# Kernel tuning notes

Measured on AMD Instinct MI355X. Metric: run time of the kernel, lower is better.

## Reference

```python
import jax, jax.numpy as jnp
import numpy as np

B, L, C, H = 2, 2048, 1024, 16
D = C // H  # dim per head

def setup_inputs() -> dict:
    key = jax.random.key(0)
    ks = jax.random.split(key, 13)
    s = 1.0 / np.sqrt(C)
    inp = {
        "query": jax.random.normal(ks[0], (B, L, C), jnp.float32),
        "key": jax.random.normal(ks[1], (B, L, C), jnp.float32),
        "value": jax.random.normal(ks[2], (B, L, C), jnp.float32),
        "mask": jax.random.randint(ks[3], (B, 1, L, L), 0, 2, jnp.int32),
        "WQ": jax.random.normal(ks[4], (C, C), jnp.float32) * s,
        "bQ": jnp.zeros((C,), jnp.float32),
        "WK": jax.random.normal(ks[5], (C, C), jnp.float32) * s,
        "bK": jnp.zeros((C,), jnp.float32),
        "WV": jax.random.normal(ks[6], (C, C), jnp.float32) * s,
        "bV": jnp.zeros((C,), jnp.float32),
        "WO": jax.random.normal(ks[7], (C, C), jnp.float32) * s,
        "bO": jnp.zeros((C,), jnp.float32),
    }
    return inp

def reference(query, key, value, mask, WQ, bQ, WK, bK, WV, bV, WO, bO):
    b = query.shape[0]
    # projections: x @ W + b  (W stored [in, out])
    Q = query @ WQ + bQ
    K = key @ WK + bK
    V = value @ WV + bV
    # [B, L, C] -> [B, H, L, D]
    def split_heads(x):
        return x.reshape(b, -1, H, D).transpose(0, 2, 1, 3)
    Qh, Kh, Vh = split_heads(Q), split_heads(K), split_heads(V)
    scores = jnp.einsum("bhqd,bhkd->bhqk", Qh, Kh) / jnp.sqrt(jnp.float32(D))
    scores = jnp.where(mask == 0, jnp.float32(-1e9), scores)
    attn = jax.nn.softmax(scores, axis=-1)
    Z = jnp.einsum("bhqk,bhkd->bhqd", attn, Vh)  # [B, H, L, D]
    Z = Z.transpose(0, 2, 1, 3).reshape(b, Q.shape[1], C)
    return Z @ WO + bO
```

## Files before the change

kernel.cpp:

```cpp
#include <hip/hip_runtime.h>

#define BB 2
#define LL 2048
#define CC 1024
#define HH 16
#define DD 64
#define MM (BB * LL)

typedef __bf16 bf16x8 __attribute__((ext_vector_type(8)));
typedef float  f32x4  __attribute__((ext_vector_type(4)));

#define LOG2E 1.44269504088896340736f
#if defined(__has_builtin)
#if __has_builtin(__builtin_amdgcn_exp2f)
#define EXP2F(x) __builtin_amdgcn_exp2f(x)
#else
#define EXP2F(x) exp2f(x)
#endif
#else
#define EXP2F(x) exp2f(x)
#endif

__device__ __forceinline__ unsigned short f2bf(float x) {
    return __builtin_bit_cast(unsigned short, (__bf16)x);
}
__device__ __forceinline__ void split2(float x, unsigned short& hi, unsigned short& lo) {
    __bf16 h = (__bf16)x;
    hi = __builtin_bit_cast(unsigned short, h);
    lo = __builtin_bit_cast(unsigned short, (__bf16)(x - (float)h));
}

#define GLOAD_LDS16(g, l)                                                      \
    __builtin_amdgcn_global_load_lds(                                          \
        (const __attribute__((address_space(1))) void*)(g),                    \
        (__attribute__((address_space(3))) void*)(l), 16, 0, 0)

#define MFMA16(a, b, c) __builtin_amdgcn_mfma_f32_16x16x32_bf16((a), (b), (c), 0, 0, 0)

__global__ __launch_bounds__(256) void w_prep(
    const float* __restrict__ W, unsigned short* __restrict__ Whi,
    unsigned short* __restrict__ Wlo)
{
    __shared__ float T[64][65];
    const int tid = threadIdx.x;
    const int k0 = blockIdx.x * 64, n0 = blockIdx.y * 64;
    #pragma unroll
    for (int p = 0; p < 4; ++p) {
        const int idx = tid + p * 256;
        const int r = idx >> 4, c4 = idx & 15;
        float4 v = *(const float4*)&W[(size_t)(k0 + r) * CC + n0 + c4 * 4];
        T[r][c4 * 4 + 0] = v.x; T[r][c4 * 4 + 1] = v.y;
        T[r][c4 * 4 + 2] = v.z; T[r][c4 * 4 + 3] = v.w;
    }
    __syncthreads();
    #pragma unroll
    for (int p = 0; p < 16; ++p) {
        const int idx = tid + p * 256;
        const int n = idx >> 6, k = idx & 63;
        unsigned short hi, lo;
        split2(T[k][n], hi, lo);
        Whi[(size_t)(n0 + n) * CC + k0 + k] = hi;
        Wlo[(size_t)(n0 + n) * CC + k0 + k] = lo;
    }
}

__global__ __launch_bounds__(256) void x_prep(
    const float* __restrict__ X, unsigned short* __restrict__ Xhi,
    unsigned short* __restrict__ Xlo)
{
    const size_t i = (size_t)blockIdx.x * 256 + threadIdx.x;
    float4 v = *(const float4*)&X[i * 4];
    unsigned short h0, l0, h1, l1, h2, l2, h3, l3;
    split2(v.x, h0, l0); split2(v.y, h1, l1);
    split2(v.z, h2, l2); split2(v.w, h3, l3);
    ushort4 hv; hv.x = h0; hv.y = h1; hv.z = h2; hv.w = h3;
    ushort4 lv; lv.x = l0; lv.y = l1; lv.z = l2; lv.w = l3;
    *(ushort4*)&Xhi[i * 4] = hv;
    *(ushort4*)&Xlo[i * 4] = lv;
}

__global__ __launch_bounds__(256) void vt_prep(
    const float* __restrict__ Vp, unsigned short* __restrict__ Vt)
{
    __shared__ float T[64][65];
    const int tid = threadIdx.x;
    const int t = blockIdx.x, h = blockIdx.y, b = blockIdx.z;
    #pragma unroll
    for (int p = 0; p < 4; ++p) {
        const int idx = tid + p * 256;
        const int r = idx >> 4, c4 = idx & 15;
        float4 v = *(const float4*)&Vp[(size_t)(b * LL + t * 64 + r) * CC + h * DD + c4 * 4];
        T[r][c4 * 4 + 0] = v.x; T[r][c4 * 4 + 1] = v.y;
        T[r][c4 * 4 + 2] = v.z; T[r][c4 * 4 + 3] = v.w;
    }
    __syncthreads();
    unsigned short* out = Vt + (size_t)(b * HH + h) * DD * LL;
    #pragma unroll
    for (int p = 0; p < 16; ++p) {
        const int idx = tid + p * 256;
        const int d = idx >> 6, l = idx & 63;
        out[(size_t)d * LL + t * 64 + l] = f2bf(T[l][d]);
    }
}

__global__ __launch_bounds__(256) void mask_pack(
    const int* __restrict__ mask, unsigned int* __restrict__ mp)
{
    const size_t wi = (size_t)blockIdx.x * 256 + threadIdx.x;
    const int* src = mask + wi * 32;
    unsigned int v = 0;
    #pragma unroll
    for (int j = 0; j < 32; j += 4) {
        int4 m4 = *(const int4*)&src[j];
        if (m4.x != 0) v |= 1u << (j + 0);
        if (m4.y != 0) v |= 1u << (j + 1);
        if (m4.z != 0) v |= 1u << (j + 2);
        if (m4.w != 0) v |= 1u << (j + 3);
    }
    mp[wi] = v;
}

template <int MODE>
__global__ __launch_bounds__(256) void gemm_split(
    const unsigned short* __restrict__ Ahi, const unsigned short* __restrict__ Alo,
    const unsigned short* __restrict__ Bhi, const unsigned short* __restrict__ Blo,
    const float* __restrict__ bias, float scale,
    float* __restrict__ Yf,
    unsigned short* __restrict__ Yhi, unsigned short* __restrict__ Ylo)
{
    __shared__ __align__(16) unsigned short Ah[2][128 * 32];
    __shared__ __align__(16) unsigned short Al[2][128 * 32];
    __shared__ __align__(16) unsigned short Bh[2][128 * 32];
    __shared__ __align__(16) unsigned short Bl[2][128 * 32];

    const int tid  = threadIdx.x;
    const int lane = tid & 63, w = tid >> 6;
    const int wr = w >> 1, wc = w & 1;
    const int lr = lane & 15, kg = lane >> 4;
    const int row0 = blockIdx.x * 128, col0 = blockIdx.y * 128;

    f32x4 acc[4][4];
    #pragma unroll
    for (int i = 0; i < 4; ++i)
        #pragma unroll
        for (int j = 0; j < 4; ++j)
            acc[i][j] = (f32x4){0.f, 0.f, 0.f, 0.f};

    const int srow = lane >> 2;
    const int ssl  = ((lane & 3) ^ ((srow >> 1) & 3)) * 8;

    #define GSTAGE(bufi, kt_)                                                  \
        {                                                                      \
            const int k0_ = (kt_) * 32;                                        \
            _Pragma("unroll")                                                  \
            for (int c = 0; c < 2; ++c) {                                      \
                const int chunk = w * 2 + c;                                   \
                const int r = chunk * 16 + srow;                               \
                GLOAD_LDS16(Ahi + (size_t)(row0 + r) * CC + k0_ + ssl, &Ah[bufi][chunk * 512]); \
                GLOAD_LDS16(Alo + (size_t)(row0 + r) * CC + k0_ + ssl, &Al[bufi][chunk * 512]); \
                GLOAD_LDS16(Bhi + (size_t)(col0 + r) * CC + k0_ + ssl, &Bh[bufi][chunk * 512]); \
                GLOAD_LDS16(Blo + (size_t)(col0 + r) * CC + k0_ + ssl, &Bl[bufi][chunk * 512]); \
            }                                                                  \
        }

    GSTAGE(0, 0);
    __syncthreads();

    const int NT = CC / 32;
    for (int kt = 0; kt < NT; ++kt) {
        const int cur = kt & 1;
        if (kt + 1 < NT) GSTAGE(cur ^ 1, kt + 1);

        bf16x8 ah[4], al[4], bh[4], bl[4];
        const int ko = (kg ^ ((lr >> 1) & 3)) * 8;
        #pragma unroll
        for (int i = 0; i < 4; ++i) {
            ah[i] = *(const bf16x8*)&Ah[cur][(wr * 64 + i * 16 + lr) * 32 + ko];
            al[i] = *(const bf16x8*)&Al[cur][(wr * 64 + i * 16 + lr) * 32 + ko];
            bh[i] = *(const bf16x8*)&Bh[cur][(wc * 64 + i * 16 + lr) * 32 + ko];
            bl[i] = *(const bf16x8*)&Bl[cur][(wc * 64 + i * 16 + lr) * 32 + ko];
        }
        #pragma unroll
        for (int i = 0; i < 4; ++i)
            #pragma unroll
            for (int j = 0; j < 4; ++j) {
                acc[i][j] = MFMA16(ah[i], bh[j], acc[i][j]);
                acc[i][j] = MFMA16(ah[i], bl[j], acc[i][j]);
                acc[i][j] = MFMA16(al[i], bh[j], acc[i][j]);
            }
        __syncthreads();
    }
    #undef GSTAGE

    #pragma unroll
    for (int j = 0; j < 4; ++j) {
        const int n = col0 + wc * 64 + j * 16 + lr;
        const float bv = bias[n];
        #pragma unroll
        for (int i = 0; i < 4; ++i) {
            const int mbase = row0 + wr * 64 + i * 16 + kg * 4;
            #pragma unroll
            for (int r = 0; r < 4; ++r) {
                const float v = (acc[i][j][r] + bv) * scale;
                const int m = mbase + r;
                if (MODE == 0) {
                    Yf[(size_t)m * CC + n] = v;
                } else {
                    const int bb = m >> 11, ll = m & (LL - 1);
                    const int hh = n >> 6, dd = n & 63;
                    const size_t o = ((size_t)(bb * HH + hh) * LL + ll) * DD + dd;
                    unsigned short hi, lo;
                    split2(v, hi, lo);
                    Yhi[o] = hi; Ylo[o] = lo;
                }
            }
        }
    }
}

__global__ __launch_bounds__(256) void flash_mfma(
    const unsigned short* __restrict__ Qhi, const unsigned short* __restrict__ Qlo,
    const unsigned short* __restrict__ Khi, const unsigned short* __restrict__ Klo,
    const unsigned short* __restrict__ Vt,  const unsigned int* __restrict__ maskp,
    unsigned short* __restrict__ Zhi, unsigned short* __restrict__ Zlo)
{
    __shared__ __align__(16) unsigned short Kh_s[2][64 * 64];
    __shared__ __align__(16) unsigned short Kl_s[2][64 * 64];
    __shared__ __align__(16) unsigned short Vt_s[2][64 * 64];
    __shared__ __align__(16) __bf16 Ps[4][16 * 72];

    const int tid  = threadIdx.x;
    const int lane = tid & 63, w = tid >> 6;
    const int lr = lane & 15, kg = lane >> 4;
    const int q0 = blockIdx.x * 64;
    const int h = blockIdx.y, b = blockIdx.z;
    const size_t bh = (size_t)(b * HH + h);

    const unsigned short* Qhi_b = Qhi + bh * LL * DD;
    const unsigned short* Qlo_b = Qlo + bh * LL * DD;
    const unsigned short* Khi_b = Khi + bh * LL * DD;
    const unsigned short* Klo_b = Klo + bh * LL * DD;
    const unsigned short* Vt_b  = Vt  + bh * DD * LL;

    const int qrow = q0 + w * 16 + lr;
    bf16x8 qh[2], ql[2];
    #pragma unroll
    for (int s = 0; s < 2; ++s) {
        qh[s] = *(const bf16x8*)&Qhi_b[(size_t)qrow * DD + s * 32 + kg * 8];
        ql[s] = *(const bf16x8*)&Qlo_b[(size_t)qrow * DD + s * 32 + kg * 8];
    }

    f32x4 oacc[4];
    float m_r[4], l_r[4];
    #pragma unroll
    for (int r = 0; r < 4; ++r) {
        oacc[r] = (f32x4){0.f, 0.f, 0.f, 0.f};
        m_r[r] = -3.0e38f; l_r[r] = 0.f;
    }

    #define FSTAGE(bufi, kt_)                                                  \
        {                                                                      \
            _Pragma("unroll")                                                  \
            for (int c = 0; c < 2; ++c) {                                      \
                const int chunk = w * 2 + c;                                   \
                const int rowi = chunk * 8 + (lane >> 3);                      \
                const int cb   = (lane & 7) * 16;                              \
                const int scb  = cb ^ ((rowi & 7) << 4);                       \
                GLOAD_LDS16(Khi_b + (size_t)((kt_) * 64 + rowi) * DD + scb / 2, &Kh_s[bufi][chunk * 512]); \
                GLOAD_LDS16(Klo_b + (size_t)((kt_) * 64 + rowi) * DD + scb / 2, &Kl_s[bufi][chunk * 512]); \
                GLOAD_LDS16(Vt_b + (size_t)rowi * LL + (kt_) * 64 + scb / 2,    &Vt_s[bufi][chunk * 512]); \
            }                                                                  \
        }

    FSTAGE(0, 0);
    __syncthreads();

    const int NT = LL / 64;
    for (int kt = 0; kt < NT; ++kt) {
        const int cur = kt & 1;
        if (kt + 1 < NT) FSTAGE(cur ^ 1, kt + 1);

        f32x4 sacc[4];
        #pragma unroll
        for (int j = 0; j < 4; ++j) sacc[j] = (f32x4){0.f, 0.f, 0.f, 0.f};
        __builtin_amdgcn_s_setprio(1);
        #pragma unroll
        for (int j = 0; j < 4; ++j) {
            const int krow = j * 16 + lr;
            const int rswz = (krow & 7) << 4;
            #pragma unroll
            for (int s = 0; s < 2; ++s) {
                const int cb = (s * 64 + kg * 16) ^ rswz;
                bf16x8 kh = *(const bf16x8*)((const char*)&Kh_s[cur][0] + krow * 128 + cb);
                bf16x8 kl = *(const bf16x8*)((const char*)&Kl_s[cur][0] + krow * 128 + cb);
                sacc[j] = MFMA16(qh[s], kh, sacc[j]);
                sacc[j] = MFMA16(qh[s], kl, sacc[j]);
                sacc[j] = MFMA16(ql[s], kh, sacc[j]);
            }
        }
        __builtin_amdgcn_s_setprio(0);

        float mxr[4];
        #pragma unroll
        for (int r = 0; r < 4; ++r) {
            const int qr = q0 + w * 16 + kg * 4 + r;
            const unsigned int* mb = maskp + ((size_t)b * LL + qr) * (LL / 32) + kt * 2;
            const unsigned int m0 = mb[0], m1 = mb[1];
            float mx = -3.0e38f;
            #pragma unroll
            for (int j = 0; j < 4; ++j) {
                const unsigned int wsel = (j < 2) ? m0 : m1;
                const int bit = (j & 1) * 16 + lr;
                if (((wsel >> bit) & 1u) == 0u) sacc[j][r] = -1.0e9f;
                mx = fmaxf(mx, sacc[j][r]);
            }
            #pragma unroll
            for (int off = 1; off < 16; off <<= 1)
                mx = fmaxf(mx, __shfl_xor(mx, off, 16));
            mxr[r] = mx;
        }

        const float g = fmaxf(fmaxf(mxr[0] - m_r[0], mxr[1] - m_r[1]),
                              fmaxf(mxr[2] - m_r[2], mxr[3] - m_r[3]));
        if (!__all(g <= 8.0f)) {
            #pragma unroll
            for (int r = 0; r < 4; ++r) {
                const float mnew = fmaxf(m_r[r], mxr[r]);
                const float f = EXP2F(m_r[r] - mnew);
                m_r[r] = mnew;
                l_r[r] *= f;
                #pragma unroll
                for (int jd = 0; jd < 4; ++jd) oacc[jd][r] *= f;
            }
        }

        #pragma unroll
        for (int r = 0; r < 4; ++r) {
            float sum = 0.f;
            #pragma unroll
            for (int j = 0; j < 4; ++j) {
                const float p = EXP2F(sacc[j][r] - m_r[r]);
                sum += p;
                Ps[w][(kg * 4 + r) * 72 + j * 16 + lr] = (__bf16)p;
            }
            #pragma unroll
            for (int off = 1; off < 16; off <<= 1)
                sum += __shfl_xor(sum, off, 16);
            l_r[r] += sum;
        }

        __builtin_amdgcn_s_setprio(1);
        #pragma unroll
        for (int s = 0; s < 2; ++s) {
            bf16x8 pa = *(const bf16x8*)&Ps[w][lr * 72 + s * 32 + kg * 8];
            #pragma unroll
            for (int jd = 0; jd < 4; ++jd) {
                const int vrow = jd * 16 + lr;
                const int cb = (s * 64 + kg * 16) ^ ((vrow & 7) << 4);
                bf16x8 vb = *(const bf16x8*)((const char*)&Vt_s[cur][0] + vrow * 128 + cb);
                oacc[jd] = MFMA16(pa, vb, oacc[jd]);
            }
        }
        __builtin_amdgcn_s_setprio(0);
        __syncthreads();
    }
    #undef FSTAGE

    #pragma unroll
    for (int r = 0; r < 4; ++r) {
        const float inv = 1.0f / l_r[r];
        const int qg = q0 + w * 16 + kg * 4 + r;
        const size_t rowb = ((size_t)(b * LL + qg)) * CC + h * DD;
        #pragma unroll
        for (int jd = 0; jd < 4; ++jd) {
            unsigned short hi, lo;
            split2(oacc[jd][r] * inv, hi, lo);
            Zhi[rowb + jd * 16 + lr] = hi;
            Zlo[rowb + jd * 16 + lr] = lo;
        }
    }
}

extern "C" void kernel_launch(void* const* d_in, const int* in_sizes, int n_in,
                              void* d_out, int out_size, void* d_ws, size_t ws_size,
                              hipStream_t stream)
{
    const float* query = (const float*)d_in[0];
    const float* key   = (const float*)d_in[1];
    const float* value = (const float*)d_in[2];
    const int*   mask  = (const int*)d_in[3];
    const float* WQ = (const float*)d_in[4];
    const float* bQ = (const float*)d_in[5];
    const float* WK = (const float*)d_in[6];
    const float* bK = (const float*)d_in[7];
    const float* WV = (const float*)d_in[8];
    const float* bV = (const float*)d_in[9];
    const float* WO = (const float*)d_in[10];
    const float* bO = (const float*)d_in[11];
    float* out = (float*)d_out;

    char* ws = (char*)d_ws;
    const size_t MB = 1024 * 1024;
    unsigned short* WQt_hi = (unsigned short*)(ws + 0 * MB);
    unsigned short* WQt_lo = (unsigned short*)(ws + 2 * MB);
    unsigned short* WKt_hi = (unsigned short*)(ws + 4 * MB);
    unsigned short* WKt_lo = (unsigned short*)(ws + 6 * MB);
    unsigned short* WVt_hi = (unsigned short*)(ws + 8 * MB);
    unsigned short* WVt_lo = (unsigned short*)(ws + 10 * MB);
    unsigned short* WOt_hi = (unsigned short*)(ws + 12 * MB);
    unsigned short* WOt_lo = (unsigned short*)(ws + 14 * MB);
    unsigned short* Xhi    = (unsigned short*)(ws + 16 * MB);
    unsigned short* Xlo    = (unsigned short*)(ws + 24 * MB);
    unsigned short* Qh_hi  = (unsigned short*)(ws + 32 * MB);
    unsigned short* Qh_lo  = (unsigned short*)(ws + 40 * MB);
    unsigned short* Kh_hi  = (unsigned short*)(ws + 48 * MB);
    unsigned short* Kh_lo  = (unsigned short*)(ws + 56 * MB);
    float*          Vp     = (float*)(ws + 64 * MB);
    unsigned short* Vt     = (unsigned short*)(ws + 80 * MB);
    unsigned int*   maskp  = (unsigned int*)(ws + 88 * MB);

    const dim3 blk(256);
    const dim3 wgrid(CC / 64, CC / 64);
    w_prep<<<wgrid, blk, 0, stream>>>(WQ, WQt_hi, WQt_lo);
    w_prep<<<wgrid, blk, 0, stream>>>(WK, WKt_hi, WKt_lo);
    w_prep<<<wgrid, blk, 0, stream>>>(WV, WVt_hi, WVt_lo);
    w_prep<<<wgrid, blk, 0, stream>>>(WO, WOt_hi, WOt_lo);
    mask_pack<<<dim3((BB * LL * (LL / 32)) / 256), blk, 0, stream>>>(mask, maskp);

    const dim3 ggrid(MM / 128, CC / 128);
    const dim3 xgrid((size_t)MM * CC / 4 / 256);

    x_prep<<<xgrid, blk, 0, stream>>>(query, Xhi, Xlo);
    gemm_split<1><<<ggrid, blk, 0, stream>>>(Xhi, Xlo, WQt_hi, WQt_lo, bQ,
                                             0.125f * LOG2E, nullptr, Qh_hi, Qh_lo);
    x_prep<<<xgrid, blk, 0, stream>>>(key, Xhi, Xlo);
    gemm_split<1><<<ggrid, blk, 0, stream>>>(Xhi, Xlo, WKt_hi, WKt_lo, bK, 1.0f,
                                             nullptr, Kh_hi, Kh_lo);
    x_prep<<<xgrid, blk, 0, stream>>>(value, Xhi, Xlo);
    gemm_split<0><<<ggrid, blk, 0, stream>>>(Xhi, Xlo, WVt_hi, WVt_lo, bV, 1.0f,
                                             Vp, nullptr, nullptr);
    vt_prep<<<dim3(LL / 64, HH, BB), blk, 0, stream>>>(Vp, Vt);

    flash_mfma<<<dim3(LL / 64, HH, BB), blk, 0, stream>>>(
        Qh_hi, Qh_lo, Kh_hi, Kh_lo, Vt, maskp, Xhi, Xlo);

    gemm_split<0><<<ggrid, blk, 0, stream>>>(Xhi, Xlo, WOt_hi, WOt_lo, bO, 1.0f,
                                             out, nullptr, nullptr);
}
```

Baseline: 523.4 us.

## Replace double-buffered LDS staging with single-buffer load-sync-compute loops

Removes the double-buffered prefetch in both the split-bf16 GEMM and the flash attention kernel. Each iteration now loads its tile into a single LDS buffer, synchronizes, then computes. This halves LDS use per block, which may allow more resident blocks per CU. In exchange, global-to-LDS loads no longer overlap with MFMA compute inside a block, so the kernels rely on occupancy to hide memory latency.

```diff
diff --git a/kernel.cpp b/kernel.cpp
--- a/kernel.cpp
+++ b/kernel.cpp
@@ -128,10 +128,10 @@
     float* __restrict__ Yf,
     unsigned short* __restrict__ Yhi, unsigned short* __restrict__ Ylo)
 {
-    __shared__ __align__(16) unsigned short Ah[2][128 * 32];
-    __shared__ __align__(16) unsigned short Al[2][128 * 32];
-    __shared__ __align__(16) unsigned short Bh[2][128 * 32];
-    __shared__ __align__(16) unsigned short Bl[2][128 * 32];
+    __shared__ __align__(16) unsigned short Ah[128 * 32];
+    __shared__ __align__(16) unsigned short Al[128 * 32];
+    __shared__ __align__(16) unsigned short Bh[128 * 32];
+    __shared__ __align__(16) unsigned short Bl[128 * 32];
 
     const int tid  = threadIdx.x;
     const int lane = tid & 63, w = tid >> 6;
@@ -148,37 +148,29 @@
 
     const int srow = lane >> 2;
     const int ssl  = ((lane & 3) ^ ((srow >> 1) & 3)) * 8;
-
-    #define GSTAGE(bufi, kt_)                                                  \
-        {                                                                      \
-            const int k0_ = (kt_) * 32;                                        \
-            _Pragma("unroll")                                                  \
-            for (int c = 0; c < 2; ++c) {                                      \
-                const int chunk = w * 2 + c;                                   \
-                const int r = chunk * 16 + srow;                               \
-                GLOAD_LDS16(Ahi + (size_t)(row0 + r) * CC + k0_ + ssl, &Ah[bufi][chunk * 512]); \
-                GLOAD_LDS16(Alo + (size_t)(row0 + r) * CC + k0_ + ssl, &Al[bufi][chunk * 512]); \
-                GLOAD_LDS16(Bhi + (size_t)(col0 + r) * CC + k0_ + ssl, &Bh[bufi][chunk * 512]); \
-                GLOAD_LDS16(Blo + (size_t)(col0 + r) * CC + k0_ + ssl, &Bl[bufi][chunk * 512]); \
-            }                                                                  \
-        }
-
-    GSTAGE(0, 0);
-    __syncthreads();
+    const int ko   = (kg ^ ((lr >> 1) & 3)) * 8;
 
     const int NT = CC / 32;
     for (int kt = 0; kt < NT; ++kt) {
-        const int cur = kt & 1;
-        if (kt + 1 < NT) GSTAGE(cur ^ 1, kt + 1);
+        const int k0 = kt * 32;
+        #pragma unroll
+        for (int c = 0; c < 2; ++c) {
+            const int chunk = w * 2 + c;
+            const int r = chunk * 16 + srow;
+            GLOAD_LDS16(Ahi + (size_t)(row0 + r) * CC + k0 + ssl, &Ah[chunk * 512]);
+            GLOAD_LDS16(Alo + (size_t)(row0 + r) * CC + k0 + ssl, &Al[chunk * 512]);
+            GLOAD_LDS16(Bhi + (size_t)(col0 + r) * CC + k0 + ssl, &Bh[chunk * 512]);
+            GLOAD_LDS16(Blo + (size_t)(col0 + r) * CC + k0 + ssl, &Bl[chunk * 512]);
+        }
+        __syncthreads();
 
         bf16x8 ah[4], al[4], bh[4], bl[4];
-        const int ko = (kg ^ ((lr >> 1) & 3)) * 8;
         #pragma unroll
         for (int i = 0; i < 4; ++i) {
-            ah[i] = *(const bf16x8*)&Ah[cur][(wr * 64 + i * 16 + lr) * 32 + ko];
-            al[i] = *(const bf16x8*)&Al[cur][(wr * 64 + i * 16 + lr) * 32 + ko];
-            bh[i] = *(const bf16x8*)&Bh[cur][(wc * 64 + i * 16 + lr) * 32 + ko];
-            bl[i] = *(const bf16x8*)&Bl[cur][(wc * 64 + i * 16 + lr) * 32 + ko];
+            ah[i] = *(const bf16x8*)&Ah[(wr * 64 + i * 16 + lr) * 32 + ko];
+            al[i] = *(const bf16x8*)&Al[(wr * 64 + i * 16 + lr) * 32 + ko];
+            bh[i] = *(const bf16x8*)&Bh[(wc * 64 + i * 16 + lr) * 32 + ko];
+            bl[i] = *(const bf16x8*)&Bl[(wc * 64 + i * 16 + lr) * 32 + ko];
         }
         #pragma unroll
         for (int i = 0; i < 4; ++i)
@@ -190,7 +182,6 @@
             }
         __syncthreads();
     }
-    #undef GSTAGE
 
     #pragma unroll
     for (int j = 0; j < 4; ++j) {
@@ -224,9 +215,9 @@
     const unsigned short* __restrict__ Vt,  const unsigned int* __restrict__ maskp,
     unsigned short* __restrict__ Zhi, unsigned short* __restrict__ Zlo)
 {
-    __shared__ __align__(16) unsigned short Kh_s[2][64 * 64];
-    __shared__ __align__(16) unsigned short Kl_s[2][64 * 64];
-    __shared__ __align__(16) unsigned short Vt_s[2][64 * 64];
+    __shared__ __align__(16) unsigned short Kh_s[64 * 64];
+    __shared__ __align__(16) unsigned short Kl_s[64 * 64];
+    __shared__ __align__(16) unsigned short Vt_s[64 * 64];
     __shared__ __align__(16) __bf16 Ps[4][16 * 72];
 
     const int tid  = threadIdx.x;
@@ -258,27 +249,19 @@
         m_r[r] = -3.0e38f; l_r[r] = 0.f;
     }
 
-    #define FSTAGE(bufi, kt_)                                                  \
-        {                                                                      \
-            _Pragma("unroll")                                                  \
-            for (int c = 0; c < 2; ++c) {                                      \
-                const int chunk = w * 2 + c;                                   \
-                const int rowi = chunk * 8 + (lane >> 3);                      \
-                const int cb   = (lane & 7) * 16;                              \
-                const int scb  = cb ^ ((rowi & 7) << 4);                       \
-                GLOAD_LDS16(Khi_b + (size_t)((kt_) * 64 + rowi) * DD + scb / 2, &Kh_s[bufi][chunk * 512]); \
-                GLOAD_LDS16(Klo_b + (size_t)((kt_) * 64 + rowi) * DD + scb / 2, &Kl_s[bufi][chunk * 512]); \
-                GLOAD_LDS16(Vt_b + (size_t)rowi * LL + (kt_) * 64 + scb / 2,    &Vt_s[bufi][chunk * 512]); \
-            }                                                                  \
-        }
-
-    FSTAGE(0, 0);
-    __syncthreads();
-
     const int NT = LL / 64;
     for (int kt = 0; kt < NT; ++kt) {
-        const int cur = kt & 1;
-        if (kt + 1 < NT) FSTAGE(cur ^ 1, kt + 1);
+        #pragma unroll
+        for (int c = 0; c < 2; ++c) {
+            const int chunk = w * 2 + c;
+            const int rowi = chunk * 8 + (lane >> 3);
+            const int cb   = (lane & 7) * 16;
+            const int scb  = cb ^ ((rowi & 7) << 4);
+            GLOAD_LDS16(Khi_b + (size_t)(kt * 64 + rowi) * DD + scb / 2, &Kh_s[chunk * 512]);
+            GLOAD_LDS16(Klo_b + (size_t)(kt * 64 + rowi) * DD + scb / 2, &Kl_s[chunk * 512]);
+            GLOAD_LDS16(Vt_b + (size_t)rowi * LL + kt * 64 + scb / 2,    &Vt_s[chunk * 512]);
+        }
+        __syncthreads();
 
         f32x4 sacc[4];
         #pragma unroll
@@ -291,8 +274,8 @@
             #pragma unroll
             for (int s = 0; s < 2; ++s) {
                 const int cb = (s * 64 + kg * 16) ^ rswz;
-                bf16x8 kh = *(const bf16x8*)((const char*)&Kh_s[cur][0] + krow * 128 + cb);
-                bf16x8 kl = *(const bf16x8*)((const char*)&Kl_s[cur][0] + krow * 128 + cb);
+                bf16x8 kh = *(const bf16x8*)((const char*)&Kh_s[0] + krow * 128 + cb);
+                bf16x8 kl = *(const bf16x8*)((const char*)&Kl_s[0] + krow * 128 + cb);
                 sacc[j] = MFMA16(qh[s], kh, sacc[j]);
                 sacc[j] = MFMA16(qh[s], kl, sacc[j]);
                 sacc[j] = MFMA16(ql[s], kh, sacc[j]);
@@ -357,14 +340,13 @@
             for (int jd = 0; jd < 4; ++jd) {
                 const int vrow = jd * 16 + lr;
                 const int cb = (s * 64 + kg * 16) ^ ((vrow & 7) << 4);
-                bf16x8 vb = *(const bf16x8*)((const char*)&Vt_s[cur][0] + vrow * 128 + cb);
+                bf16x8 vb = *(const bf16x8*)((const char*)&Vt_s[0] + vrow * 128 + cb);
                 oacc[jd] = MFMA16(pa, vb, oacc[jd]);
             }
         }
         __builtin_amdgcn_s_setprio(0);
         __syncthreads();
     }
-    #undef FSTAGE
 
     #pragma unroll
     for (int r = 0; r < 4; ++r) {
```

Result: faster. 483.9 us (-7.5%).
